# Kernel optimization log

Hardware: AMD Instinct MI355X
Metric: run time of the kernel (lower is better)

Reference implementation:

```python
import jax, jax.numpy as jnp
import numpy as np

NUM_CLASS = 22  # restypes_with_x_and_gap


def setup_inputs() -> dict:
    key = jax.random.key(0)
    k1, k2, k3, k4 = jax.random.split(key, 4)
    b, m, n, c = 1, 128, 256, NUM_CLASS
    variant = jax.random.randint(k1, (b, m, n), 0, c)              # int variant sequences
    variant_mask = jnp.ones((b, m, n), dtype=jnp.float32)
    eij = jax.random.normal(k2, (b, n, n, c, c), dtype=jnp.float32) * 0.1  # Potts couplings wij
    ei = jax.random.normal(k3, (b, n, c), dtype=jnp.float32) * 0.1         # fields bi
    mask_vec = jnp.ones((c,), dtype=jnp.float32).at[-1].set(0.0)   # mask out gap '-' class
    sigma = jnp.ones((1,), dtype=jnp.float32)                      # prior_w=1.0, task_num=1
    return {"variant": variant, "variant_mask": variant_mask, "eij": eij,
            "ei": ei, "mask_vec": mask_vec, "sigma": sigma}


def reference(variant, variant_mask, eij, ei, mask_vec, sigma):
    c = mask_vec.shape[0]
    onehot = jax.nn.one_hot(variant, c, dtype=eij.dtype)           # [b,m,n,c]
    # fold class mask into couplings, then Potts energy per position/class
    em = eij * mask_vec                                            # [b,i,j,c,d]
    hi = jnp.einsum('bmjd,bijcd->bmic', onehot, em)                # [b,m,i,c]
    motifs = ei[:, None] + hi                                      # [b,m,i,c]
    # log_softmax=False branch: pick the logit of the active class per position
    logits = jnp.einsum('bmic,bmic->bmi', motifs, onehot)          # [b,m,i]
    # eval path: delta vs reference variant (index 0), sum-pooled, scaled by sigma
    vm = variant_mask[..., None]                                   # [b,m,i,1]
    vm = vm * vm[:, :1]
    vlogit = logits - logits[:, :1]                                # [b,m,i]
    pooled = jnp.sum(vlogit[..., None] * vm, axis=-2)              # [b,m,task_num]
    variant_logit = sigma * pooled
    return motifs, logits, variant_logit
```

## Files before the change

kernel.cpp:

```cpp
#include <hip/hip_runtime.h>

#define NC    22
#define NROW  (NC*NC)
#define NJ    256
#define NI    256
#define NM    128
#define JG    8
#define NQJ   4
#define JQ    (NJ/NQJ)
#define SS    (JQ/JG)
#define ROWDW 16
#define JROW  (NC*ROWDW)
#define TILEDW (JG*JROW)
#define F4PS  (JG*NROW/4)
#define SLAB  (NI*NM*NC)

typedef __attribute__((ext_vector_type(8))) short short8;
typedef __attribute__((ext_vector_type(4))) float f32x4;

__device__ __forceinline__ uint32_t pk_bf16(float lo, float hi) {
    uint32_t r;
    asm("v_cvt_pk_bf16_f32 %0, %1, %2" : "=v"(r) : "v"(lo), "v"(hi));
    return r;
}

__global__ __launch_bounds__(256) void potts_mfma(
    const int*   __restrict__ variant,
    const float* __restrict__ eij,
    const float* __restrict__ mask_vec,
    float*       __restrict__ part)
{
    const int i    = blockIdx.x;
    const int jq   = blockIdx.y;
    const int tid  = threadIdx.x;
    const int lane = tid & 63;
    const int wv   = tid >> 6;
    const int q    = lane >> 4;
    const int nl   = lane & 15;

    __shared__ uint32_t tile[2][TILEDW];
    __shared__ int      vtab[2][JG][NM];

    for (int p = tid; p < 2 * JG * NC * 5; p += 256) {
        const int b  = p / (JG * NC * 5), r = p % (JG * NC * 5);
        const int jl = r / (NC * 5),     r2 = r % (NC * 5);
        tile[b][jl * JROW + (r2 / 5) * ROWDW + 11 + r2 % 5] = 0;
    }

    int   l0[4], l1[4];
    float mk[4][4];
    bool  act[4];
    #pragma unroll
    for (int r = 0; r < 4; ++r) {
        const int f4 = r * 256 + tid;
        act[r] = (f4 < F4PS);
        const int fc = act[r] ? f4 : 0;
        const int jl = fc / 121, r4 = fc % 121;
        const int f2a = 2 * r4, f2b = f2a + 1;
        const int ca = f2a / 11, wa = f2a % 11;
        const int cb = f2b / 11, wb = f2b % 11;
        l0[r] = jl * JROW + ca * ROWDW + wa;
        l1[r] = jl * JROW + cb * ROWDW + wb;
        mk[r][0] = mask_vec[2 * wa];  mk[r][1] = mask_vec[2 * wa + 1];
        mk[r][2] = mask_vec[2 * wb];  mk[r][3] = mask_vec[2 * wb + 1];
    }

    const float4* gsrc = (const float4*)eij + (size_t)(i * NJ + jq * JQ) * 121;

    const int c1   = 16 + nl;
    const int off0 = nl * ROWDW + q * 4;
    const int off1 = (c1 < NC ? c1 : 0) * ROWDW + q * 4;
    const int m0a  = wv * 16;
    const int m0b  = wv * 16 + 64;

    f32x4 acc_a0 = {0.f,0.f,0.f,0.f}, acc_a1 = {0.f,0.f,0.f,0.f};
    f32x4 acc_b0 = {0.f,0.f,0.f,0.f}, acc_b1 = {0.f,0.f,0.f,0.f};

    float4 pf[4];
    int    vr[4];
    #pragma unroll
    for (int r = 0; r < 4; ++r)
        if (act[r]) pf[r] = gsrc[r * 256 + tid];
    #pragma unroll
    for (int r = 0; r < 4; ++r) {
        const int t = r * 256 + tid;
        vr[r] = variant[(t >> 3) * NJ + jq * JQ + (t & 7)];
    }

    for (int s = 0; s < SS; ++s) {
        const int bsel = s & 1;
        uint32_t* buf = tile[bsel];

        #pragma unroll
        for (int r = 0; r < 4; ++r) {
            if (act[r]) {
                const float4 v = pf[r];
                buf[l0[r]] = pk_bf16(v.x * mk[r][0], v.y * mk[r][1]);
                buf[l1[r]] = pk_bf16(v.z * mk[r][2], v.w * mk[r][3]);
            }
        }
        #pragma unroll
        for (int r = 0; r < 4; ++r) {
            const int t = r * 256 + tid;
            vtab[bsel][t & 7][t >> 3] = vr[r];
        }
        __syncthreads();

        if (s + 1 < SS) {
            const float4* gn = gsrc + (size_t)(s + 1) * F4PS;
            #pragma unroll
            for (int r = 0; r < 4; ++r)
                if (act[r]) pf[r] = gn[r * 256 + tid];
            #pragma unroll
            for (int r = 0; r < 4; ++r) {
                const int t = r * 256 + tid;
                vr[r] = variant[(t >> 3) * NJ + jq * JQ + (s + 1) * JG + (t & 7)];
            }
        }

        #pragma unroll
        for (int jl = 0; jl < JG; ++jl) {
            const uint32_t* jrow = buf + jl * JROW;
            const short8 bf0 = *(const short8*)(jrow + off0);
            const short8 bf1 = *(const short8*)(jrow + off1);

            const int va = vtab[bsel][jl][m0a + nl];
            const int vb = vtab[bsel][jl][m0b + nl];

            const uint32_t pa = 0x3F80u << ((va & 1) << 4);
            const uint32_t pb = 0x3F80u << ((vb & 1) << 4);
            const int ha = va >> 1, hb = vb >> 1, kb = q * 4;
            union { uint32_t u[4]; short8 s; } fa, fb;
            #pragma unroll
            for (int t = 0; t < 4; ++t) {
                fa.u[t] = (ha == kb + t) ? pa : 0u;
                fb.u[t] = (hb == kb + t) ? pb : 0u;
            }

            acc_a0 = __builtin_amdgcn_mfma_f32_16x16x32_bf16(fa.s, bf0, acc_a0, 0, 0, 0);
            acc_a1 = __builtin_amdgcn_mfma_f32_16x16x32_bf16(fa.s, bf1, acc_a1, 0, 0, 0);
            acc_b0 = __builtin_amdgcn_mfma_f32_16x16x32_bf16(fb.s, bf0, acc_b0, 0, 0, 0);
            acc_b1 = __builtin_amdgcn_mfma_f32_16x16x32_bf16(fb.s, bf1, acc_b1, 0, 0, 0);
        }
    }

    float* pbase = part + ((size_t)jq * NI + i) * NM * NC;
    #pragma unroll
    for (int t = 0; t < 4; ++t) {
        const int ra = m0a + q * 4 + t, rb = m0b + q * 4 + t;
        pbase[ra * NC + nl] = acc_a0[t];
        pbase[rb * NC + nl] = acc_b0[t];
        if (c1 < NC) {
            pbase[ra * NC + c1] = acc_a1[t];
            pbase[rb * NC + c1] = acc_b1[t];
        }
    }
}

__global__ __launch_bounds__(1024) void potts_reduce(
    const float* __restrict__ part,
    const int*   __restrict__ variant,
    const float* __restrict__ ei,
    float*       __restrict__ out_motifs,
    float*       __restrict__ out_logits)
{
    const int idx = blockIdx.x * 1024 + threadIdx.x;
    float s = 0.f;
    #pragma unroll
    for (int qq = 0; qq < NQJ; ++qq)
        s += part[(size_t)qq * SLAB + idx];

    const int i = idx / (NM * NC);
    const int r = idx - i * (NM * NC);
    const int m = r / NC;
    const int c = r - m * NC;

    const float v = s + ei[i * NC + c];
    out_motifs[((size_t)m * NI + i) * NC + c] = v;
    if (c == variant[m * NJ + i])
        out_logits[m * NI + i] = v;
}

__global__ __launch_bounds__(64) void potts_pool(
    const float* __restrict__ logits,
    const float* __restrict__ vmask,
    const float* __restrict__ sigma,
    float*       __restrict__ out_vl)
{
    const int m    = blockIdx.x;
    const int lane = threadIdx.x;
    float s = 0.f;
    #pragma unroll
    for (int qq = 0; qq < 4; ++qq) {
        const int i = lane + 64 * qq;
        const float vl = logits[m * NI + i] - logits[i];
        s += vl * vmask[m * NI + i] * vmask[i];
    }
    #pragma unroll
    for (int off = 32; off > 0; off >>= 1)
        s += __shfl_down(s, off, 64);
    if (lane == 0) out_vl[m] = sigma[0] * s;
}

extern "C" void kernel_launch(void* const* d_in, const int* in_sizes, int n_in,
                              void* d_out, int out_size, void* d_ws, size_t ws_size,
                              hipStream_t stream) {
    const int*   variant  = (const int*)  d_in[0];
    const float* vmask    = (const float*)d_in[1];
    const float* eij      = (const float*)d_in[2];
    const float* ei       = (const float*)d_in[3];
    const float* mask_vec = (const float*)d_in[4];
    const float* sigma    = (const float*)d_in[5];

    float* out        = (float*)d_out;
    float* out_motifs = out;
    float* out_logits = out_motifs + NM * NI * NC;
    float* out_vl     = out_logits + NM * NI;

    float* part = (float*)d_ws;

    dim3 gridA(NI, NQJ);
    potts_mfma<<<gridA, 256, 0, stream>>>(variant, eij, mask_vec, part);
    potts_reduce<<<SLAB / 1024, 1024, 0, stream>>>(part, variant, ei,
                                                   out_motifs, out_logits);
    potts_pool<<<NM, 64, 0, stream>>>(out_logits, vmask, sigma, out_vl);
}
```

Baseline: 206.4 us.

## Deepen eij prefetch, preload variant table, fuse pooling into reduce

```diff
diff --git a/kernel.cpp b/kernel.cpp
--- a/kernel.cpp
+++ b/kernel.cpp
@@ -14,6 +14,7 @@
 #define TILEDW (JG*JROW)
 #define F4PS  (JG*NROW/4)
 #define SLAB  (NI*NM*NC)
+#define NRB   (SLAB/1024)
 
 typedef __attribute__((ext_vector_type(8))) short short8;
 typedef __attribute__((ext_vector_type(4))) float f32x4;
@@ -28,7 +29,8 @@
     const int*   __restrict__ variant,
     const float* __restrict__ eij,
     const float* __restrict__ mask_vec,
-    float*       __restrict__ part)
+    float*       __restrict__ part,
+    unsigned*    __restrict__ sync_cnt)
 {
     const int i    = blockIdx.x;
     const int jq   = blockIdx.y;
@@ -38,13 +40,19 @@
     const int q    = lane >> 4;
     const int nl   = lane & 15;
 
-    __shared__ uint32_t tile[2][TILEDW];
-    __shared__ int      vtab[2][JG][NM];
+    if (i == 0 && jq == 0 && tid == 0) *sync_cnt = 0;
+
+    __shared__ uint32_t      tile[2][TILEDW];
+    __shared__ unsigned char vt8[JQ][NM];
 
     for (int p = tid; p < 2 * JG * NC * 5; p += 256) {
         const int b  = p / (JG * NC * 5), r = p % (JG * NC * 5);
         const int jl = r / (NC * 5),     r2 = r % (NC * 5);
         tile[b][jl * JROW + (r2 / 5) * ROWDW + 11 + r2 % 5] = 0;
+    }
+    for (int p = tid; p < JQ * NM; p += 256) {
+        const int m = p >> 6, jl = p & 63;
+        vt8[jl][m] = (unsigned char)variant[m * NJ + jq * JQ + jl];
     }
 
     int   l0[4], l1[4];
@@ -76,21 +84,16 @@
     f32x4 acc_a0 = {0.f,0.f,0.f,0.f}, acc_a1 = {0.f,0.f,0.f,0.f};
     f32x4 acc_b0 = {0.f,0.f,0.f,0.f}, acc_b1 = {0.f,0.f,0.f,0.f};
 
-    float4 pf[4];
-    int    vr[4];
+    float4 pfA[4], pfB[4];
     #pragma unroll
     for (int r = 0; r < 4; ++r)
-        if (act[r]) pf[r] = gsrc[r * 256 + tid];
-    #pragma unroll
-    for (int r = 0; r < 4; ++r) {
-        const int t = r * 256 + tid;
-        vr[r] = variant[(t >> 3) * NJ + jq * JQ + (t & 7)];
-    }
-
-    for (int s = 0; s < SS; ++s) {
-        const int bsel = s & 1;
+        if (act[r]) pfA[r] = gsrc[r * 256 + tid];
+    #pragma unroll
+    for (int r = 0; r < 4; ++r)
+        if (act[r]) pfB[r] = gsrc[(size_t)F4PS + r * 256 + tid];
+
+    auto step = [&](float4 (&pf)[4], int bsel, int s) {
         uint32_t* buf = tile[bsel];
-
         #pragma unroll
         for (int r = 0; r < 4; ++r) {
             if (act[r]) {
@@ -99,23 +102,12 @@
                 buf[l1[r]] = pk_bf16(v.z * mk[r][2], v.w * mk[r][3]);
             }
         }
-        #pragma unroll
-        for (int r = 0; r < 4; ++r) {
-            const int t = r * 256 + tid;
-            vtab[bsel][t & 7][t >> 3] = vr[r];
-        }
         __syncthreads();
-
-        if (s + 1 < SS) {
-            const float4* gn = gsrc + (size_t)(s + 1) * F4PS;
+        if (s + 2 < SS) {
+            const float4* gn = gsrc + (size_t)(s + 2) * F4PS;
             #pragma unroll
             for (int r = 0; r < 4; ++r)
                 if (act[r]) pf[r] = gn[r * 256 + tid];
-            #pragma unroll
-            for (int r = 0; r < 4; ++r) {
-                const int t = r * 256 + tid;
-                vr[r] = variant[(t >> 3) * NJ + jq * JQ + (s + 1) * JG + (t & 7)];
-            }
         }
 
         #pragma unroll
@@ -124,8 +116,9 @@
             const short8 bf0 = *(const short8*)(jrow + off0);
             const short8 bf1 = *(const short8*)(jrow + off1);
 
-            const int va = vtab[bsel][jl][m0a + nl];
-            const int vb = vtab[bsel][jl][m0b + nl];
+            const unsigned char* vrow = vt8[s * JG + jl];
+            const int va = vrow[m0a + nl];
+            const int vb = vrow[m0b + nl];
 
             const uint32_t pa = 0x3F80u << ((va & 1) << 4);
             const uint32_t pb = 0x3F80u << ((vb & 1) << 4);
@@ -142,6 +135,11 @@
             acc_b0 = __builtin_amdgcn_mfma_f32_16x16x32_bf16(fb.s, bf0, acc_b0, 0, 0, 0);
             acc_b1 = __builtin_amdgcn_mfma_f32_16x16x32_bf16(fb.s, bf1, acc_b1, 0, 0, 0);
         }
+    };
+
+    for (int s = 0; s < SS; s += 2) {
+        step(pfA, 0, s);
+        step(pfB, 1, s + 1);
     }
 
     float* pbase = part + ((size_t)jq * NI + i) * NM * NC;
@@ -161,8 +159,12 @@
     const float* __restrict__ part,
     const int*   __restrict__ variant,
     const float* __restrict__ ei,
+    const float* __restrict__ vmask,
+    const float* __restrict__ sigma,
     float*       __restrict__ out_motifs,
-    float*       __restrict__ out_logits)
+    float*       __restrict__ out_logits,
+    float*       __restrict__ out_vl,
+    unsigned*    __restrict__ sync_cnt)
 {
     const int idx = blockIdx.x * 1024 + threadIdx.x;
     float s = 0.f;
@@ -179,27 +181,28 @@
     out_motifs[((size_t)m * NI + i) * NC + c] = v;
     if (c == variant[m * NJ + i])
         out_logits[m * NI + i] = v;
-}
-
-__global__ __launch_bounds__(64) void potts_pool(
-    const float* __restrict__ logits,
-    const float* __restrict__ vmask,
-    const float* __restrict__ sigma,
-    float*       __restrict__ out_vl)
-{
-    const int m    = blockIdx.x;
-    const int lane = threadIdx.x;
-    float s = 0.f;
-    #pragma unroll
-    for (int qq = 0; qq < 4; ++qq) {
-        const int i = lane + 64 * qq;
-        const float vl = logits[m * NI + i] - logits[i];
-        s += vl * vmask[m * NI + i] * vmask[i];
-    }
-    #pragma unroll
-    for (int off = 32; off > 0; off >>= 1)
-        s += __shfl_down(s, off, 64);
-    if (lane == 0) out_vl[m] = sigma[0] * s;
+
+    __shared__ unsigned ticket;
+    __threadfence();
+    __syncthreads();
+    if (threadIdx.x == 0) ticket = atomicAdd(sync_cnt, 1u);
+    __syncthreads();
+    if (ticket == NRB - 1) {
+        __threadfence();
+        const int t   = threadIdx.x;
+        const int mm  = t >> 3, sub = t & 7;
+        float acc = 0.f;
+        #pragma unroll 4
+        for (int k = 0; k < 32; ++k) {
+            const int ii = sub * 32 + k;
+            const float vl = out_logits[mm * NI + ii] - out_logits[ii];
+            acc += vl * vmask[mm * NI + ii] * vmask[ii];
+        }
+        acc += __shfl_down(acc, 4, 8);
+        acc += __shfl_down(acc, 2, 8);
+        acc += __shfl_down(acc, 1, 8);
+        if (sub == 0) out_vl[mm] = sigma[0] * acc;
+    }
 }
 
 extern "C" void kernel_launch(void* const* d_in, const int* in_sizes, int n_in,
@@ -217,11 +220,12 @@
     float* out_logits = out_motifs + NM * NI * NC;
     float* out_vl     = out_logits + NM * NI;
 
-    float* part = (float*)d_ws;
+    float*    part     = (float*)d_ws;
+    unsigned* sync_cnt = (unsigned*)(part + (size_t)NQJ * SLAB);
 
     dim3 gridA(NI, NQJ);
-    potts_mfma<<<gridA, 256, 0, stream>>>(variant, eij, mask_vec, part);
-    potts_reduce<<<SLAB / 1024, 1024, 0, stream>>>(part, variant, ei,
-                                                   out_motifs, out_logits);
-    potts_pool<<<NM, 64, 0, stream>>>(out_logits, vmask, sigma, out_vl);
-}
+    potts_mfma<<<gridA, 256, 0, stream>>>(variant, eij, mask_vec, part, sync_cnt);
+    potts_reduce<<<NRB, 1024, 0, stream>>>(part, variant, ei, vmask, sigma,
+                                           out_motifs, out_logits, out_vl,
+                                           sync_cnt);
+}
```

After: 465.2 us. 2.25x slower.

## Give each wave private j-slices, fold class mask into one-hot, reduce waves in LDS

Applied to the files above, without the earlier changes.

```diff
diff --git a/kernel.cpp b/kernel.cpp
--- a/kernel.cpp
+++ b/kernel.cpp
@@ -5,18 +5,24 @@
 #define NJ    256
 #define NI    256
 #define NM    128
-#define JG    8
 #define NQJ   4
 #define JQ    (NJ/NQJ)
-#define SS    (JQ/JG)
+#define SS    8
 #define ROWDW 16
 #define JROW  (NC*ROWDW)
-#define TILEDW (JG*JROW)
-#define F4PS  (JG*NROW/4)
+#define WBUF  (2*JROW)
+#define VTS   132
 #define SLAB  (NI*NM*NC)
+#define NRB   (SLAB/1024)
 
 typedef __attribute__((ext_vector_type(8))) short short8;
 typedef __attribute__((ext_vector_type(4))) float f32x4;
+
+__device__ __forceinline__ uint32_t bf16rne(float x) {
+    uint32_t u = __float_as_uint(x);
+    u += 0x7FFFu + ((u >> 16) & 1u);
+    return u >> 16;
+}
 
 __device__ __forceinline__ uint32_t pk_bf16(float lo, float hi) {
     uint32_t r;
@@ -24,7 +30,7 @@
     return r;
 }
 
-__global__ __launch_bounds__(256) void potts_mfma(
+__global__ __launch_bounds__(256, 4) void potts_mfma(
     const int*   __restrict__ variant,
     const float* __restrict__ eij,
     const float* __restrict__ mask_vec,
@@ -34,126 +40,135 @@
     const int jq   = blockIdx.y;
     const int tid  = threadIdx.x;
     const int lane = tid & 63;
-    const int wv   = tid >> 6;
+    const int w    = tid >> 6;
     const int q    = lane >> 4;
     const int nl   = lane & 15;
-
-    __shared__ uint32_t tile[2][TILEDW];
-    __shared__ int      vtab[2][JG][NM];
-
-    for (int p = tid; p < 2 * JG * NC * 5; p += 256) {
-        const int b  = p / (JG * NC * 5), r = p % (JG * NC * 5);
-        const int jl = r / (NC * 5),     r2 = r % (NC * 5);
-        tile[b][jl * JROW + (r2 / 5) * ROWDW + 11 + r2 % 5] = 0;
-    }
-
-    int   l0[4], l1[4];
-    float mk[4][4];
-    bool  act[4];
+    const int kb   = q * 4;
+
+    __shared__ uint32_t      tile[4][WBUF * 2];
+    __shared__ unsigned char vt8[JQ * VTS];
+    __shared__ uint32_t      patTab[32];
+
+    if (tid < 32) {
+        const uint32_t mb = (tid < NC) ? bf16rne(mask_vec[tid]) : 0u;
+        patTab[tid] = mb << ((tid & 1) << 4);
+    }
+    for (int p = tid; p < JQ * NM; p += 256) {
+        const int jl = p & 63, m = p >> 6;
+        vt8[jl * VTS + m] = (unsigned char)variant[m * NJ + jq * JQ + jl];
+    }
+    {
+        uint32_t* wbase = tile[w];
+        for (int p = lane; p < 2 * 2 * NC * 5; p += 64) {
+            const int b = p / (2 * NC * 5), r = p % (2 * NC * 5);
+            const int jl = r / (NC * 5), r2 = r % (NC * 5);
+            wbase[b * WBUF + jl * JROW + (r2 / 5) * ROWDW + 11 + r2 % 5] = 0;
+        }
+    }
+    __syncthreads();
+
+    int  l0[4], l1[4];
+    bool act[4];
     #pragma unroll
     for (int r = 0; r < 4; ++r) {
-        const int f4 = r * 256 + tid;
-        act[r] = (f4 < F4PS);
+        const int f4 = r * 64 + lane;
+        act[r] = (f4 < 242);
         const int fc = act[r] ? f4 : 0;
         const int jl = fc / 121, r4 = fc % 121;
         const int f2a = 2 * r4, f2b = f2a + 1;
-        const int ca = f2a / 11, wa = f2a % 11;
-        const int cb = f2b / 11, wb = f2b % 11;
-        l0[r] = jl * JROW + ca * ROWDW + wa;
-        l1[r] = jl * JROW + cb * ROWDW + wb;
-        mk[r][0] = mask_vec[2 * wa];  mk[r][1] = mask_vec[2 * wa + 1];
-        mk[r][2] = mask_vec[2 * wb];  mk[r][3] = mask_vec[2 * wb + 1];
-    }
-
-    const float4* gsrc = (const float4*)eij + (size_t)(i * NJ + jq * JQ) * 121;
+        l0[r] = jl * JROW + (f2a / 11) * ROWDW + f2a % 11;
+        l1[r] = jl * JROW + (f2b / 11) * ROWDW + f2b % 11;
+    }
+
+    const float4* gsrc = (const float4*)eij
+                       + (size_t)(i * NJ + jq * JQ + w * 16) * (NROW / 4);
 
     const int c1   = 16 + nl;
-    const int off0 = nl * ROWDW + q * 4;
-    const int off1 = (c1 < NC ? c1 : 0) * ROWDW + q * 4;
-    const int m0a  = wv * 16;
-    const int m0b  = wv * 16 + 64;
-
-    f32x4 acc_a0 = {0.f,0.f,0.f,0.f}, acc_a1 = {0.f,0.f,0.f,0.f};
-    f32x4 acc_b0 = {0.f,0.f,0.f,0.f}, acc_b1 = {0.f,0.f,0.f,0.f};
+    const int off0 = nl * ROWDW + kb;
+    const int off1 = (c1 < NC ? c1 : 0) * ROWDW + kb;
+
+    f32x4 acc[8][2];
+    #pragma unroll
+    for (int t = 0; t < 8; ++t) {
+        acc[t][0] = (f32x4){0.f, 0.f, 0.f, 0.f};
+        acc[t][1] = (f32x4){0.f, 0.f, 0.f, 0.f};
+    }
 
     float4 pf[4];
-    int    vr[4];
     #pragma unroll
     for (int r = 0; r < 4; ++r)
-        if (act[r]) pf[r] = gsrc[r * 256 + tid];
-    #pragma unroll
-    for (int r = 0; r < 4; ++r) {
-        const int t = r * 256 + tid;
-        vr[r] = variant[(t >> 3) * NJ + jq * JQ + (t & 7)];
-    }
+        if (act[r]) pf[r] = gsrc[r * 64 + lane];
 
     for (int s = 0; s < SS; ++s) {
-        const int bsel = s & 1;
-        uint32_t* buf = tile[bsel];
+        uint32_t* buf = tile[w] + (s & 1) * WBUF;
 
         #pragma unroll
         for (int r = 0; r < 4; ++r) {
             if (act[r]) {
                 const float4 v = pf[r];
-                buf[l0[r]] = pk_bf16(v.x * mk[r][0], v.y * mk[r][1]);
-                buf[l1[r]] = pk_bf16(v.z * mk[r][2], v.w * mk[r][3]);
-            }
-        }
-        #pragma unroll
-        for (int r = 0; r < 4; ++r) {
-            const int t = r * 256 + tid;
-            vtab[bsel][t & 7][t >> 3] = vr[r];
-        }
-        __syncthreads();
-
+                buf[l0[r]] = pk_bf16(v.x, v.y);
+                buf[l1[r]] = pk_bf16(v.z, v.w);
+            }
+        }
         if (s + 1 < SS) {
-            const float4* gn = gsrc + (size_t)(s + 1) * F4PS;
+            const float4* gn = gsrc + (size_t)(s + 1) * 242;
             #pragma unroll
             for (int r = 0; r < 4; ++r)
-                if (act[r]) pf[r] = gn[r * 256 + tid];
-            #pragma unroll
-            for (int r = 0; r < 4; ++r) {
-                const int t = r * 256 + tid;
-                vr[r] = variant[(t >> 3) * NJ + jq * JQ + (s + 1) * JG + (t & 7)];
-            }
-        }
-
-        #pragma unroll
-        for (int jl = 0; jl < JG; ++jl) {
-            const uint32_t* jrow = buf + jl * JROW;
+                if (act[r]) pf[r] = gn[r * 64 + lane];
+        }
+
+        #pragma unroll
+        for (int jj = 0; jj < 2; ++jj) {
+            const uint32_t* jrow = buf + jj * JROW;
             const short8 bf0 = *(const short8*)(jrow + off0);
             const short8 bf1 = *(const short8*)(jrow + off1);
 
-            const int va = vtab[bsel][jl][m0a + nl];
-            const int vb = vtab[bsel][jl][m0b + nl];
-
-            const uint32_t pa = 0x3F80u << ((va & 1) << 4);
-            const uint32_t pb = 0x3F80u << ((vb & 1) << 4);
-            const int ha = va >> 1, hb = vb >> 1, kb = q * 4;
-            union { uint32_t u[4]; short8 s; } fa, fb;
-            #pragma unroll
-            for (int t = 0; t < 4; ++t) {
-                fa.u[t] = (ha == kb + t) ? pa : 0u;
-                fb.u[t] = (hb == kb + t) ? pb : 0u;
-            }
-
-            acc_a0 = __builtin_amdgcn_mfma_f32_16x16x32_bf16(fa.s, bf0, acc_a0, 0, 0, 0);
-            acc_a1 = __builtin_amdgcn_mfma_f32_16x16x32_bf16(fa.s, bf1, acc_a1, 0, 0, 0);
-            acc_b0 = __builtin_amdgcn_mfma_f32_16x16x32_bf16(fb.s, bf0, acc_b0, 0, 0, 0);
-            acc_b1 = __builtin_amdgcn_mfma_f32_16x16x32_bf16(fb.s, bf1, acc_b1, 0, 0, 0);
-        }
-    }
-
-    float* pbase = part + ((size_t)jq * NI + i) * NM * NC;
-    #pragma unroll
-    for (int t = 0; t < 4; ++t) {
-        const int ra = m0a + q * 4 + t, rb = m0b + q * 4 + t;
-        pbase[ra * NC + nl] = acc_a0[t];
-        pbase[rb * NC + nl] = acc_b0[t];
-        if (c1 < NC) {
-            pbase[ra * NC + c1] = acc_a1[t];
-            pbase[rb * NC + c1] = acc_b1[t];
-        }
+            const unsigned char* vrow = &vt8[(w * 16 + s * 2 + jj) * VTS];
+            #pragma unroll
+            for (int t = 0; t < 8; ++t) {
+                const int      va = vrow[t * 16 + nl];
+                const uint32_t pa = patTab[va];
+                const int      ha = va >> 1;
+                union { uint32_t u[4]; short8 s; } fa;
+                #pragma unroll
+                for (int tt = 0; tt < 4; ++tt)
+                    fa.u[tt] = (ha == kb + tt) ? pa : 0u;
+                acc[t][0] = __builtin_amdgcn_mfma_f32_16x16x32_bf16(fa.s, bf0, acc[t][0], 0, 0, 0);
+                acc[t][1] = __builtin_amdgcn_mfma_f32_16x16x32_bf16(fa.s, bf1, acc[t][1], 0, 0, 0);
+            }
+        }
+    }
+
+    __syncthreads();
+    float* red   = (float*)&tile[0][0];
+    float* myred = red + (w & 1) * (NM * NC);
+    if (w < 2) {
+        #pragma unroll
+        for (int t = 0; t < 8; ++t)
+            #pragma unroll
+            for (int tt = 0; tt < 4; ++tt) {
+                const int m = t * 16 + kb + tt;
+                myred[m * NC + nl] = acc[t][0][tt];
+                if (c1 < NC) myred[m * NC + c1] = acc[t][1][tt];
+            }
+    }
+    __syncthreads();
+    if (w >= 2) {
+        #pragma unroll
+        for (int t = 0; t < 8; ++t)
+            #pragma unroll
+            for (int tt = 0; tt < 4; ++tt) {
+                const int m = t * 16 + kb + tt;
+                myred[m * NC + nl] += acc[t][0][tt];
+                if (c1 < NC) myred[m * NC + c1] += acc[t][1][tt];
+            }
+    }
+    __syncthreads();
+    float* pbase = part + ((size_t)jq * NI + i) * (NM * NC);
+    #pragma unroll
+    for (int k = 0; k < 11; ++k) {
+        const int p = k * 256 + tid;
+        pbase[p] = red[p] + red[NM * NC + p];
     }
 }
 
@@ -221,7 +236,7 @@
 
     dim3 gridA(NI, NQJ);
     potts_mfma<<<gridA, 256, 0, stream>>>(variant, eij, mask_vec, part);
-    potts_reduce<<<SLAB / 1024, 1024, 0, stream>>>(part, variant, ei,
-                                                   out_motifs, out_logits);
+    potts_reduce<<<NRB, 1024, 0, stream>>>(part, variant, ei,
+                                           out_motifs, out_logits);
     potts_pool<<<NM, 64, 0, stream>>>(out_logits, vmask, sigma, out_vl);
 }
```

After: 210.4 us. No clear change (+2.0%).
